# Kernel optimization log

Measured on AMD Instinct MI355X. Metric: run time of the kernel, lower is better.

## Reference

```python
import jax, jax.numpy as jnp
import numpy as np

B, F_IN, D_IN = 1024, 64, 64
N_CAPS, D_CAPS = 32, 64
ROUTINGS = 3
HEADS = 2
EPS = 1e-7  # K.epsilon()


def setup_inputs() -> dict:
    key = jax.random.key(0)
    ks = jax.random.split(key, 8)
    P = N_CAPS * (N_CAPS - 1) // 2
    return {
        "x": jax.random.normal(ks[0], (B, F_IN, D_IN), jnp.float32),
        "reweight_W": jax.random.normal(ks[1], (D_IN, N_CAPS, D_CAPS), jnp.float32) * 0.05,
        "routing_init": 10.0 * jax.random.truncated_normal(ks[2], -2.0, 2.0, (N_CAPS, F_IN), jnp.float32),
        "kernel_fm": jnp.full((N_CAPS, 1), 0.5, jnp.float32),
        "bias_fm": jnp.zeros((D_CAPS,), jnp.float32),
        "kernel_mf": jnp.ones((P, 1), jnp.float32),
        "bias_mf": jnp.zeros((D_CAPS,), jnp.float32),
        "kernel_highint": jnp.full((N_CAPS, 1), 0.5, jnp.float32),
        "bias_highint": jnp.zeros((D_CAPS * HEADS,), jnp.float32),
        "W_query": jax.random.normal(ks[3], (D_CAPS, D_CAPS * HEADS), jnp.float32) * 0.05,
        "W_key": jax.random.normal(ks[4], (D_CAPS, D_CAPS * HEADS), jnp.float32) * 0.05,
        "W_value": jax.random.normal(ks[5], (D_CAPS, D_CAPS * HEADS), jnp.float32) * 0.05,
        "W_res": jax.random.normal(ks[6], (D_CAPS, D_CAPS * HEADS), jnp.float32) * 0.05,
    }


def _squash(v):
    s = jnp.sum(v * v, axis=-1, keepdims=True) + EPS
    return (jnp.sqrt(s) / (0.5 + s)) * v


def _heads(t):
    # [B,N,H*F] -> [H,B,N,F] (matches tf.stack(tf.split(t, H, axis=2)))
    b, n, _ = t.shape
    return t.reshape(b, n, HEADS, D_CAPS).transpose(2, 0, 1, 3)


def reference(x, reweight_W, routing_init, kernel_fm, bias_fm, kernel_mf, bias_mf,
              kernel_highint, bias_highint, W_query, W_key, W_value, W_res):
    # inputs_hat: [B, N, F, C]
    inputs_hat = jnp.einsum('bfd,dnc->bnfc', x, reweight_W)
    b_logits = jnp.broadcast_to(routing_init[None], (x.shape[0], N_CAPS, F_IN))
    for _ in range(ROUTINGS):
        c = jax.nn.softmax(b_logits, axis=1)            # softmax over capsules
        outputs = _squash(jnp.einsum('bnf,bnfc->bnc', c, inputs_hat))
        b_logits = b_logits + jnp.einsum('bnc,bnfc->bnf', outputs, inputs_hat)
    c = jax.nn.softmax(b_logits, axis=1)
    routing_score = c[..., None]                        # [B,N,F,1]
    attention_output = routing_score * inputs_hat       # [B,N,F,C]

    # FM per-field: square-of-sum minus sum-of-square over input capsules
    sum_f = jnp.sum(attention_output, axis=2)           # [B,N,C]
    field_fm = sum_f ** 2 - jnp.sum(attention_output ** 2, axis=2)
    hi_fm = jnp.sum(field_fm * kernel_fm[None], axis=1) + bias_fm  # [B,C]

    field_wise_vectors = sum_f                          # [B,N,C]

    # pairwise MF interactions (itertools.combinations order == triu indices)
    li, ri = np.triu_indices(N_CAPS, k=1)
    emb_prod = field_wise_vectors[:, li] * field_wise_vectors[:, ri]  # [B,P,C]
    h_mf = jnp.sum(emb_prod * kernel_mf[None], axis=1) + bias_mf      # [B,C]

    # InteractingLayer (multi-head self-attention over fields, use_res=True)
    q = _heads(jnp.einsum('bnd,de->bne', field_wise_vectors, W_query))  # [H,B,N,F]
    k = _heads(jnp.einsum('bnd,de->bne', field_wise_vectors, W_key))
    v = _heads(jnp.einsum('bnd,de->bne', field_wise_vectors, W_value))
    attn = jax.nn.softmax(jnp.einsum('hbnf,hbmf->hbnm', q, k), axis=-1)
    out = jnp.einsum('hbnm,hbmf->hbnf', attn, v)        # [H,B,N,F]
    out = out.transpose(1, 2, 0, 3).reshape(x.shape[0], N_CAPS, HEADS * D_CAPS)
    res = jnp.einsum('bnd,de->bne', field_wise_vectors, W_res)
    fv2 = jax.nn.relu(out + res)                        # [B,N,H*F]
    high_int = jnp.sum(fv2 * kernel_highint[None], axis=1) + bias_highint  # [B,2C]

    return jnp.concatenate([hi_fm, h_mf, high_int], axis=-1), routing_score
```

## Files before the change

kernel.cpp:

```cpp
#include <hip/hip_runtime.h>


#define EPS_SQ 1e-7f

typedef __attribute__((ext_vector_type(8))) short bf16x8;
typedef __attribute__((ext_vector_type(4))) float floatx4;

__device__ __forceinline__ int lidx(int r, int c) {
  return r * 68 + ((((c >> 2) ^ (r >> 2)) & 15) << 2) + (c & 3);
}
__device__ __forceinline__ int lidx64(int r, int c) {
  return r * 64 + ((((c >> 2) ^ r ^ (r >> 2)) & 15) << 2) + (c & 3);
}
__device__ __forceinline__ unsigned short f2bf(float f) {
  unsigned u = __float_as_uint(f);
  u += 0x7FFFu + ((u >> 16) & 1u);
  return (unsigned short)(u >> 16);
}

__global__ __launch_bounds__(256) void k_prep2(
    const float* __restrict__ W, const float* __restrict__ Wq,
    const float* __restrict__ Wk, const float* __restrict__ kmf,
    float* __restrict__ Qb, float* __restrict__ Ab, float* __restrict__ Kb)
{
  const int t = threadIdx.x;
  if (blockIdx.x < 32) {
    __shared__ __align__(16) float Mn[64 * 68];
    const int n = blockIdx.x;
#pragma unroll
    for (int k = 0; k < 4; k++) {
      int lin = t + 256 * k; int d = lin >> 4; int c0 = (lin & 15) << 2;
      *(float4*)&Mn[lidx(d, c0)] = *(const float4*)(W + d * 2048 + n * 64 + c0);
    }
    __syncthreads();
    const int d1 = (t >> 4) * 4, d2 = (t & 15) * 4;
    float acc[4][4] = {};
    for (int cq = 0; cq < 64; cq += 4) {
      float m1[4][4], m2[4][4];
#pragma unroll
      for (int i = 0; i < 4; i++) *(float4*)m1[i] = *(const float4*)&Mn[lidx(d1 + i, cq)];
#pragma unroll
      for (int j = 0; j < 4; j++) *(float4*)m2[j] = *(const float4*)&Mn[lidx(d2 + j, cq)];
#pragma unroll
      for (int i = 0; i < 4; i++)
#pragma unroll
        for (int j = 0; j < 4; j++) {
          float s = 0.f;
#pragma unroll
          for (int k = 0; k < 4; k++) s += m1[i][k] * m2[j][k];
          acc[i][j] += s;
        }
    }
#pragma unroll
    for (int i = 0; i < 4; i++)
      *(float4*)(Qb + n * 4096 + (d1 + i) * 64 + d2) = *(float4*)acc[i];
  } else if (blockIdx.x < 40) {
    __shared__ __align__(16) float wkS[64 * 68];
    __shared__ __align__(16) float wqS[16 * 68];
    const int hb = blockIdx.x - 32;
    const int h = hb & 1, rg = hb >> 1;
#pragma unroll
    for (int k = 0; k < 4; k++) {
      int lin = t + 256 * k; int dp = lin >> 4; int e0 = (lin & 15) << 2;
      *(float4*)&wkS[lidx(dp, e0)] = *(const float4*)(Wk + dp * 128 + h * 64 + e0);
    }
    {
      int dl = t >> 4, e0 = (t & 15) << 2;
      *(float4*)&wqS[lidx(dl, e0)] = *(const float4*)(Wq + (rg * 16 + dl) * 128 + h * 64 + e0);
    }
    __syncthreads();
    const int dl = t >> 4, dp0 = (t & 15) << 2;
    float acc[4] = {};
    for (int e = 0; e < 64; e += 4) {
      float q4[4];
      *(float4*)q4 = *(const float4*)&wqS[lidx(dl, e)];
#pragma unroll
      for (int c = 0; c < 4; c++) {
        float mr[4];
        *(float4*)mr = *(const float4*)&wkS[lidx(dp0 + c, e)];
        acc[c] += q4[0] * mr[0] + q4[1] * mr[1] + q4[2] * mr[2] + q4[3] * mr[3];
      }
    }
    *(float4*)(Ab + h * 4096 + (rg * 16 + dl) * 64 + dp0) = *(float4*)acc;
  } else {
    __shared__ float Ks[1024];
    *(float4*)&Ks[t * 4] = make_float4(0.f, 0.f, 0.f, 0.f);
    __syncthreads();
    if (t < 248) {
#pragma unroll
      for (int j = 0; j < 2; j++) {
        int p = t * 2 + j;
        if (p < 496) {
          int l = 0, rem = p;
          while (rem >= 31 - l) { rem -= 31 - l; ++l; }
          int r = l + 1 + rem;
          float v = kmf[p];
          Ks[l * 32 + r] = v;
          Ks[r * 32 + l] = v;
        }
      }
    }
    __syncthreads();
    *(float4*)&Kb[t * 4] = *(const float4*)&Ks[t * 4];
  }
}

__global__ __launch_bounds__(512, 4) void k_route3(
    const float* __restrict__ x, const float* __restrict__ W,
    const float* __restrict__ rinit, const float* __restrict__ Qb,
    float* __restrict__ rs, float* __restrict__ fwv)
{
  __shared__ __align__(16) float smem[2 * 10240];

  const int t = threadIdx.x;
  const int tb = t >> 8, tt = t & 255;
  const int b = blockIdx.x * 2 + tb;

  float* xs  = smem + tb * 10240;
  float* bS  = smem + tb * 10240 + 4096;
  float* cOw = smem + tb * 10240 + 6144;
  float* xcS = smem + tb * 10240 + 8192;

  float* xc0 = smem + 8192;
  float* xc1 = smem + 10240 + 8192;
  float* ow0 = smem + 6144;
  float* ow1 = smem + 10240 + 6144;

#pragma unroll
  for (int k = 0; k < 4; k++) {
    int lin = tt + 256 * k; int f = lin >> 4; int d0 = (lin & 15) << 2;
    *(float4*)&xs[lidx64(f, d0)] = *(const float4*)(x + b * 4096 + f * 64 + d0);
  }
#pragma unroll
  for (int k = 0; k < 2; k++) {
    int lin = tt + 256 * k; int n = lin >> 4; int f0 = (lin & 15) << 2;
    *(float4*)&bS[lidx64(n, f0)] = *(const float4*)(rinit + n * 64 + f0);
  }
  __syncthreads();

  const int tn = tt >> 4, tlo = tt & 15;
  const int nq = t >> 4, sub = t & 15;

  for (int it = 0; it < 4; it++) {
    {
      const int nl = tt & 31, fg = tt >> 5;
#pragma unroll
      for (int qq = 0; qq < 2; qq++) {
        const int f0 = (fg * 2 + qq) * 4;
        float v[4];
        *(float4*)v = *(const float4*)&bS[lidx64(nl, f0)];
        float e[4];
#pragma unroll
        for (int j = 0; j < 4; j++) {
          float m = v[j];
          m = fmaxf(m, __shfl_xor(m, 16, 64));
          m = fmaxf(m, __shfl_xor(m, 8, 64));
          m = fmaxf(m, __shfl_xor(m, 4, 64));
          m = fmaxf(m, __shfl_xor(m, 2, 64));
          m = fmaxf(m, __shfl_xor(m, 1, 64));
          e[j] = __expf(v[j] - m);
          float s = e[j];
          s += __shfl_xor(s, 16, 64);
          s += __shfl_xor(s, 8, 64);
          s += __shfl_xor(s, 4, 64);
          s += __shfl_xor(s, 2, 64);
          s += __shfl_xor(s, 1, 64);
          e[j] /= s;
        }
        *(float4*)&cOw[lidx64(nl, f0)] = *(float4*)e;
      }
    }
    __syncthreads();
    if (it == 3) {
#pragma unroll
      for (int k = 0; k < 2; k++) {
        int lin = tt + 256 * k;
        int n = lin >> 4, fq = lin & 15;
        float4 v = *(const float4*)&cOw[lidx64(n, fq * 4)];
        *(float4*)(rs + b * 2048 + n * 64 + fq * 4) = v;
      }
    }
    {
      const int n0 = tn * 2, d0 = tlo * 4;
      float acc[2][4] = {{0, 0, 0, 0}, {0, 0, 0, 0}};
      for (int fq = 0; fq < 16; fq++) {
        float c0[4], c1[4];
        *(float4*)c0 = *(const float4*)&cOw[lidx64(n0, fq * 4)];
        *(float4*)c1 = *(const float4*)&cOw[lidx64(n0 + 1, fq * 4)];
#pragma unroll
        for (int j = 0; j < 4; j++) {
          float xr[4];
          *(float4*)xr = *(const float4*)&xs[lidx64(fq * 4 + j, d0)];
#pragma unroll
          for (int i = 0; i < 4; i++) {
            acc[0][i] += c0[j] * xr[i];
            acc[1][i] += c1[j] * xr[i];
          }
        }
      }
      *(float4*)&xcS[lidx64(n0, d0)] = *(float4*)acc[0];
      *(float4*)&xcS[lidx64(n0 + 1, d0)] = *(float4*)acc[1];
    }
    __syncthreads();
    if (it == 3) break;

    {
      const float* Qn = Qb + nq * 4096 + sub * 4;
      float y0[4] = {}, y1[4] = {};
#pragma unroll 4
      for (int dq = 0; dq < 16; dq++) {
        float xv0[4], xv1[4];
        *(float4*)xv0 = *(const float4*)&xc0[lidx64(nq, dq * 4)];
        *(float4*)xv1 = *(const float4*)&xc1[lidx64(nq, dq * 4)];
#pragma unroll
        for (int j = 0; j < 4; j++) {
          float4 q = *(const float4*)(Qn + (dq * 4 + j) * 64);
          y0[0] += xv0[j] * q.x; y0[1] += xv0[j] * q.y;
          y0[2] += xv0[j] * q.z; y0[3] += xv0[j] * q.w;
          y1[0] += xv1[j] * q.x; y1[1] += xv1[j] * q.y;
          y1[2] += xv1[j] * q.z; y1[3] += xv1[j] * q.w;
        }
      }
      float xa0[4], xa1[4];
      *(float4*)xa0 = *(const float4*)&xc0[lidx64(nq, sub * 4)];
      *(float4*)xa1 = *(const float4*)&xc1[lidx64(nq, sub * 4)];
      float ps0 = y0[0] * xa0[0] + y0[1] * xa0[1] + y0[2] * xa0[2] + y0[3] * xa0[3];
      float ps1 = y1[0] * xa1[0] + y1[1] * xa1[1] + y1[2] * xa1[2] + y1[3] * xa1[3];
      ps0 += __shfl_xor(ps0, 1, 64); ps0 += __shfl_xor(ps0, 2, 64);
      ps0 += __shfl_xor(ps0, 4, 64); ps0 += __shfl_xor(ps0, 8, 64);
      ps1 += __shfl_xor(ps1, 1, 64); ps1 += __shfl_xor(ps1, 2, 64);
      ps1 += __shfl_xor(ps1, 4, 64); ps1 += __shfl_xor(ps1, 8, 64);
      const float ss0 = ps0 + EPS_SQ, ss1 = ps1 + EPS_SQ;
      const float sc0 = sqrtf(ss0) / (0.5f + ss0);
      const float sc1 = sqrtf(ss1) / (0.5f + ss1);
      float o0[4] = {y0[0] * sc0, y0[1] * sc0, y0[2] * sc0, y0[3] * sc0};
      float o1[4] = {y1[0] * sc1, y1[1] * sc1, y1[2] * sc1, y1[3] * sc1};
      *(float4*)&ow0[lidx64(nq, sub * 4)] = *(float4*)o0;
      *(float4*)&ow1[lidx64(nq, sub * 4)] = *(float4*)o1;
    }
    __syncthreads();

    {
      const int n0 = tn * 2, f0 = tlo * 4;
      float acc[2][4] = {{0, 0, 0, 0}, {0, 0, 0, 0}};
      for (int dq = 0; dq < 64; dq += 4) {
        float o[2][4];
        *(float4*)o[0] = *(const float4*)&cOw[lidx64(n0, dq)];
        *(float4*)o[1] = *(const float4*)&cOw[lidx64(n0 + 1, dq)];
#pragma unroll
        for (int i = 0; i < 4; i++) {
          float xr[4];
          *(float4*)xr = *(const float4*)&xs[lidx64(f0 + i, dq)];
#pragma unroll
          for (int k = 0; k < 4; k++) {
            acc[0][i] += o[0][k] * xr[k];
            acc[1][i] += o[1][k] * xr[k];
          }
        }
      }
#pragma unroll
      for (int j = 0; j < 2; j++) {
        float tmp[4];
        *(float4*)tmp = *(const float4*)&bS[lidx64(n0 + j, f0)];
#pragma unroll
        for (int i = 0; i < 4; i++) tmp[i] += acc[j][i];
        *(float4*)&bS[lidx64(n0 + j, f0)] = *(float4*)tmp;
      }
    }
    __syncthreads();
  }

  {
    const float* Wn = W + nq * 64 + sub * 4;
    float a0[4] = {}, a1[4] = {};
#pragma unroll 4
    for (int dq = 0; dq < 16; dq++) {
      float xv0[4], xv1[4];
      *(float4*)xv0 = *(const float4*)&xc0[lidx64(nq, dq * 4)];
      *(float4*)xv1 = *(const float4*)&xc1[lidx64(nq, dq * 4)];
#pragma unroll
      for (int j = 0; j < 4; j++) {
        float4 w = *(const float4*)(Wn + (dq * 4 + j) * 2048);
        a0[0] += xv0[j] * w.x; a0[1] += xv0[j] * w.y;
        a0[2] += xv0[j] * w.z; a0[3] += xv0[j] * w.w;
        a1[0] += xv1[j] * w.x; a1[1] += xv1[j] * w.y;
        a1[2] += xv1[j] * w.z; a1[3] += xv1[j] * w.w;
      }
    }
    const int b0g = blockIdx.x * 2;
    *(float4*)(fwv + b0g * 2048 + nq * 64 + sub * 4) = *(float4*)a0;
    *(float4*)(fwv + (b0g + 1) * 2048 + nq * 64 + sub * 4) = *(float4*)a1;
  }
}

__global__ __launch_bounds__(256) void k_ih(
    const float* __restrict__ x, const float* __restrict__ W,
    const float* __restrict__ rs, float* __restrict__ ssq)
{
  __shared__ __align__(16) unsigned short xB[4 * 64 * 64];
  __shared__ __align__(16) unsigned short wB[2 * 64 * 64];
  __shared__ unsigned short cF2[4 * 8 * 64];
  const int n_oct = (blockIdx.x & 3) << 3, b0 = (blockIdx.x >> 2) * 4;
  const int t = threadIdx.x, w = t >> 6, lane = t & 63;

#pragma unroll
  for (int k = 0; k < 16; k++) {
    int ch = t + 256 * k;
    int bb = ch >> 10, rem = ch & 1023;
    int f = rem >> 4, fq = rem & 15;
    int dg = fq >> 1, half = fq & 1;
    float4 v = *(const float4*)(x + ((b0 + bb) * 64 + f) * 64 + fq * 4);
    unsigned p0 = f2bf(v.x) | ((unsigned)f2bf(v.y) << 16);
    unsigned p1 = f2bf(v.z) | ((unsigned)f2bf(v.w) << 16);
    *(uint2*)&xB[bb * 4096 + f * 64 + ((dg ^ (f & 7)) << 3) + half * 4] =
        make_uint2(p0, p1);
  }
#pragma unroll
  for (int nn = 0; nn < 8; nn++) {
    float v = rs[(b0 + w) * 2048 + (n_oct + nn) * 64 + lane];
    cF2[(w * 8 + nn) * 64 + lane] = f2bf(v * v);
  }
  __syncthreads();

  const int m = lane & 15, q = lane >> 4, ms = m & 7;
  bf16x8 a[4][2];
#pragma unroll
  for (int mi = 0; mi < 4; mi++) {
    const unsigned short* bp = xB + w * 4096 + (mi * 16 + m) * 64;
#pragma unroll
    for (int kk = 0; kk < 2; kk++)
      a[mi][kk] = *(const bf16x8*)&bp[((kk * 4 + q) ^ ms) << 3];
  }

  for (int np = 0; np < 4; np++) {
    const int n0 = n_oct + np * 2;
    __syncthreads();
    {
      int dd = t >> 2, cq = t & 3;
      int dg = dd >> 3, dl = dd & 7;
#pragma unroll
      for (int nn = 0; nn < 2; nn++) {
        const float* wp = W + dd * 2048 + (n0 + nn) * 64 + cq * 16;
        unsigned short* base = wB + nn * 4096;
#pragma unroll
        for (int i4 = 0; i4 < 4; i4++) {
          float4 v = *(const float4*)(wp + i4 * 4);
          float vv[4] = {v.x, v.y, v.z, v.w};
#pragma unroll
          for (int j = 0; j < 4; j++) {
            int c = cq * 16 + i4 * 4 + j;
            base[c * 64 + ((dg ^ (c & 7)) << 3) + dl] = f2bf(vv[j]);
          }
        }
      }
    }
    __syncthreads();
#pragma unroll
    for (int nn = 0; nn < 2; nn++) {
      bf16x8 bf[4][2];
#pragma unroll
      for (int ci = 0; ci < 4; ci++) {
        const unsigned short* bp = wB + nn * 4096 + (ci * 16 + m) * 64;
#pragma unroll
        for (int kk = 0; kk < 2; kk++)
          bf[ci][kk] = *(const bf16x8*)&bp[((kk * 4 + q) ^ ms) << 3];
      }
      float ps[4] = {0.f, 0.f, 0.f, 0.f};
      const unsigned short* cf = cF2 + (w * 8 + np * 2 + nn) * 64 + q * 4;
#pragma unroll
      for (int mi = 0; mi < 4; mi++) {
        float cfv[4];
#pragma unroll
        for (int r = 0; r < 4; r++)
          cfv[r] = __uint_as_float((unsigned)cf[mi * 16 + r] << 16);
#pragma unroll
        for (int ci = 0; ci < 4; ci++) {
          floatx4 c0 = {0.f, 0.f, 0.f, 0.f};
          c0 = __builtin_amdgcn_mfma_f32_16x16x32_bf16(a[mi][0], bf[ci][0], c0, 0, 0, 0);
          c0 = __builtin_amdgcn_mfma_f32_16x16x32_bf16(a[mi][1], bf[ci][1], c0, 0, 0, 0);
#pragma unroll
          for (int r = 0; r < 4; r++) { float tv = c0[r]; ps[ci] += cfv[r] * tv * tv; }
        }
      }
#pragma unroll
      for (int ci = 0; ci < 4; ci++) {
        ps[ci] += __shfl_xor(ps[ci], 16, 64);
        ps[ci] += __shfl_xor(ps[ci], 32, 64);
      }
      if (q == 0) {
#pragma unroll
        for (int ci = 0; ci < 4; ci++)
          ssq[(b0 + w) * 2048 + (n0 + nn) * 64 + ci * 16 + m] = ps[ci];
      }
    }
  }
}

__global__ __launch_bounds__(256) void k_attn(
    const float* __restrict__ fwv, const float* __restrict__ ssq,
    const float* __restrict__ Ab, const float* __restrict__ Kb,
    const float* __restrict__ Wv, const float* __restrict__ Wr,
    const float* __restrict__ kfm, const float* __restrict__ bfm,
    const float* __restrict__ bmf, const float* __restrict__ khi,
    const float* __restrict__ bhi, float* __restrict__ out0)
{
  __shared__ __align__(16) float smem[8832];
  float* fwS  = smem;
  float* pS   = smem + 2176;
  float* bufA = smem + 4480;
  float* tS   = smem + 6656;
  float* vS   = smem + 4480;
  float* redH = smem + 2176;
  float* Kf   = smem + 4480;
  float* red1 = smem + 5504;

  const int b = blockIdx.x, t = threadIdx.x;
  const int tn = t >> 4, te = t & 15;
  const int n0 = tn * 2, e0 = te * 8, d0 = te * 4;

#pragma unroll
  for (int k = 0; k < 2; k++) {
    int lin = t + 256 * k; int nn = lin >> 4; int c0 = (lin & 15) << 2;
    *(float4*)&fwS[lidx(nn, c0)] = *(const float4*)(fwv + b * 2048 + nn * 64 + c0);
  }
  __syncthreads();

  for (int h = 0; h < 2; h++) {
    float tacc[2][4] = {};
    for (int half = 0; half < 2; half++) {
#pragma unroll
      for (int k = 0; k < 2; k++) {
        int lin = t + 256 * k; int d = lin >> 4; int c0 = (lin & 15) << 2;
        *(float4*)&bufA[lidx(d, c0)] =
            *(const float4*)(Ab + h * 4096 + (half * 32 + d) * 64 + c0);
      }
      __syncthreads();
      for (int dq = 0; dq < 32; dq += 4) {
        float fw0[4], fw1[4];
        *(float4*)fw0 = *(const float4*)&fwS[lidx(n0, half * 32 + dq)];
        *(float4*)fw1 = *(const float4*)&fwS[lidx(n0 + 1, half * 32 + dq)];
#pragma unroll
        for (int j = 0; j < 4; j++) {
          float mr[4];
          *(float4*)mr = *(const float4*)&bufA[lidx(dq + j, d0)];
#pragma unroll
          for (int c = 0; c < 4; c++) {
            tacc[0][c] += fw0[j] * mr[c];
            tacc[1][c] += fw1[j] * mr[c];
          }
        }
      }
      __syncthreads();
    }
    *(float4*)&tS[lidx(n0, d0)] = *(float4*)tacc[0];
    *(float4*)&tS[lidx(n0 + 1, d0)] = *(float4*)tacc[1];
    __syncthreads();
    {
      const int m0 = te * 2;
      float s00 = 0.f, s01 = 0.f, s10 = 0.f, s11 = 0.f;
      for (int kk = 0; kk < 16; kk++) {
        float ta0[4], ta1[4], f0[4], f1[4];
        *(float4*)ta0 = *(const float4*)&tS[lidx(n0, kk * 4)];
        *(float4*)ta1 = *(const float4*)&tS[lidx(n0 + 1, kk * 4)];
        *(float4*)f0 = *(const float4*)&fwS[lidx(m0, kk * 4)];
        *(float4*)f1 = *(const float4*)&fwS[lidx(m0 + 1, kk * 4)];
#pragma unroll
        for (int j = 0; j < 4; j++) {
          s00 += ta0[j] * f0[j]; s01 += ta0[j] * f1[j];
          s10 += ta1[j] * f0[j]; s11 += ta1[j] * f1[j];
        }
      }
      pS[(h * 32 + n0) * 36 + m0] = s00;
      pS[(h * 32 + n0) * 36 + m0 + 1] = s01;
      pS[(h * 32 + n0 + 1) * 36 + m0] = s10;
      pS[(h * 32 + n0 + 1) * 36 + m0 + 1] = s11;
    }
    __syncthreads();
  }

  {
    const int r = t >> 2, sub = t & 3;
    const int base = r * 36 + sub * 8;
    float v0[4], v1[4];
    *(float4*)v0 = *(const float4*)&pS[base];
    *(float4*)v1 = *(const float4*)&pS[base + 4];
    float mx = fmaxf(fmaxf(fmaxf(v0[0], v0[1]), fmaxf(v0[2], v0[3])),
                     fmaxf(fmaxf(v1[0], v1[1]), fmaxf(v1[2], v1[3])));
    mx = fmaxf(mx, __shfl_xor(mx, 1, 64));
    mx = fmaxf(mx, __shfl_xor(mx, 2, 64));
    float sum = 0.f;
#pragma unroll
    for (int j = 0; j < 4; j++) { v0[j] = __expf(v0[j] - mx); sum += v0[j]; }
#pragma unroll
    for (int j = 0; j < 4; j++) { v1[j] = __expf(v1[j] - mx); sum += v1[j]; }
    sum += __shfl_xor(sum, 1, 64);
    sum += __shfl_xor(sum, 2, 64);
    const float inv = 1.0f / sum;
#pragma unroll
    for (int j = 0; j < 4; j++) { v0[j] *= inv; v1[j] *= inv; }
    *(float4*)&pS[base] = *(float4*)v0;
    *(float4*)&pS[base + 4] = *(float4*)v1;
  }
  __syncthreads();

  {
    float acc[2][8] = {};
    for (int dq = 0; dq < 64; dq += 4) {
      float fw0[4], fw1[4];
      *(float4*)fw0 = *(const float4*)&fwS[lidx(n0, dq)];
      *(float4*)fw1 = *(const float4*)&fwS[lidx(n0 + 1, dq)];
#pragma unroll
      for (int jj = 0; jj < 4; jj++) {
        float w8[8];
        *(float4*)&w8[0] = *(const float4*)(Wv + (dq + jj) * 128 + e0);
        *(float4*)&w8[4] = *(const float4*)(Wv + (dq + jj) * 128 + e0 + 4);
#pragma unroll
        for (int j = 0; j < 8; j++) {
          acc[0][j] += fw0[jj] * w8[j];
          acc[1][j] += fw1[jj] * w8[j];
        }
      }
    }
    *(float4*)&vS[n0 * 132 + e0] = *(float4*)&acc[0][0];
    *(float4*)&vS[n0 * 132 + e0 + 4] = *(float4*)&acc[0][4];
    *(float4*)&vS[(n0 + 1) * 132 + e0] = *(float4*)&acc[1][0];
    *(float4*)&vS[(n0 + 1) * 132 + e0 + 4] = *(float4*)&acc[1][4];
  }
  __syncthreads();

  {
    const int h2 = te >> 3;
    float pacc[2][8] = {};
    for (int m = 0; m < 32; m++) {
      float p0 = pS[(h2 * 32 + n0) * 36 + m];
      float p1 = pS[(h2 * 32 + n0 + 1) * 36 + m];
      float vr[8];
      *(float4*)&vr[0] = *(const float4*)&vS[m * 132 + e0];
      *(float4*)&vr[4] = *(const float4*)&vS[m * 132 + e0 + 4];
#pragma unroll
      for (int j = 0; j < 8; j++) {
        pacc[0][j] += p0 * vr[j];
        pacc[1][j] += p1 * vr[j];
      }
    }
    for (int dq = 0; dq < 64; dq += 4) {
      float fw0[4], fw1[4];
      *(float4*)fw0 = *(const float4*)&fwS[lidx(n0, dq)];
      *(float4*)fw1 = *(const float4*)&fwS[lidx(n0 + 1, dq)];
#pragma unroll
      for (int jj = 0; jj < 4; jj++) {
        float w8[8];
        *(float4*)&w8[0] = *(const float4*)(Wr + (dq + jj) * 128 + e0);
        *(float4*)&w8[4] = *(const float4*)(Wr + (dq + jj) * 128 + e0 + 4);
#pragma unroll
        for (int j = 0; j < 8; j++) {
          pacc[0][j] += fw0[jj] * w8[j];
          pacc[1][j] += fw1[jj] * w8[j];
        }
      }
    }
    __syncthreads();
    {
      float kh0 = khi[n0], kh1 = khi[n0 + 1];
      float ph[8];
#pragma unroll
      for (int j = 0; j < 8; j++)
        ph[j] = kh0 * fmaxf(pacc[0][j], 0.f) + kh1 * fmaxf(pacc[1][j], 0.f);
      *(float4*)&redH[tn * 132 + e0] = *(float4*)&ph[0];
      *(float4*)&redH[tn * 132 + e0 + 4] = *(float4*)&ph[4];
    }
  }
  *(float4*)&Kf[t * 4] = *(const float4*)(Kb + t * 4);
  __syncthreads();

  if (t < 128) {
    float s = 0.f;
#pragma unroll
    for (int k = 0; k < 16; k++) s += redH[k * 132 + t];
    out0[b * 256 + 128 + t] = s + bhi[t];
  }
  {
    const int c = t & 63, nq = t >> 6;
    float p = 0.f;
#pragma unroll
    for (int k = 0; k < 8; k++) {
      int nn = nq * 8 + k;
      float fv = fwS[lidx(nn, c)];
      float sv = ssq[b * 2048 + nn * 64 + c];
      p += (fv * fv - sv) * kfm[nn];
    }
    red1[nq * 68 + c] = p;
    float inner[8] = {};
    for (int r = 0; r < 32; r++) {
      float fr = fwS[lidx(r, c)];
#pragma unroll
      for (int l8 = 0; l8 < 8; l8++)
        inner[l8] += Kf[(nq * 8 + l8) * 32 + r] * fr;
    }
    float hmf = 0.f;
#pragma unroll
    for (int l8 = 0; l8 < 8; l8++)
      hmf += fwS[lidx(nq * 8 + l8, c)] * inner[l8];
    red1[(4 + nq) * 68 + c] = hmf;
  }
  __syncthreads();
  if (t < 64) {
    out0[b * 256 + t] = red1[t] + red1[68 + t] + red1[136 + t] + red1[204 + t] + bfm[t];
    float h2 = red1[272 + t] + red1[340 + t] + red1[408 + t] + red1[476 + t];
    out0[b * 256 + 64 + t] = 0.5f * h2 + bmf[t];
  }
}

extern "C" void kernel_launch(void* const* d_in, const int* in_sizes, int n_in,
                              void* d_out, int out_size, void* d_ws, size_t ws_size,
                              hipStream_t stream) {
  (void)in_sizes; (void)n_in; (void)out_size; (void)ws_size;
  const float* x     = (const float*)d_in[0];
  const float* W     = (const float*)d_in[1];
  const float* rinit = (const float*)d_in[2];
  const float* kfm   = (const float*)d_in[3];
  const float* bfm   = (const float*)d_in[4];
  const float* kmf   = (const float*)d_in[5];
  const float* bmf   = (const float*)d_in[6];
  const float* khi   = (const float*)d_in[7];
  const float* bhi   = (const float*)d_in[8];
  const float* Wq    = (const float*)d_in[9];
  const float* Wk    = (const float*)d_in[10];
  const float* Wv    = (const float*)d_in[11];
  const float* Wr    = (const float*)d_in[12];

  float* out0 = (float*)d_out;
  float* rs   = out0 + 1024 * 256;

  float* ws   = (float*)d_ws;
  float* Abuf = ws;
  float* Kbuf = ws + 8192;
  float* Qbuf = ws + 16384;
  float* fwv  = ws + 2097152;
  float* ssq  = ws + 2 * 2097152;

  k_prep2<<<41, 256, 0, stream>>>(W, Wq, Wk, kmf, Qbuf, Abuf, Kbuf);
  k_route3<<<512, 512, 0, stream>>>(x, W, rinit, Qbuf, rs, fwv);
  k_ih<<<1024, 256, 0, stream>>>(x, W, rs, ssq);
  k_attn<<<1024, 256, 0, stream>>>(fwv, ssq, Abuf, Kbuf, Wv, Wr,
                                   kfm, bfm, bmf, khi, bhi, out0);
}
```

Measured before the change: 260.1 us.

## Process four batch rows per routing block with split-K partial sums

```diff
diff --git a/kernel.cpp b/kernel.cpp
--- a/kernel.cpp
+++ b/kernel.cpp
@@ -105,26 +105,24 @@
   }
 }
 
-__global__ __launch_bounds__(512, 4) void k_route3(
+__global__ __launch_bounds__(1024) void k_route4(
     const float* __restrict__ x, const float* __restrict__ W,
     const float* __restrict__ rinit, const float* __restrict__ Qb,
     float* __restrict__ rs, float* __restrict__ fwv)
 {
-  __shared__ __align__(16) float smem[2 * 10240];
+  __shared__ __align__(16) float smem[4 * 8192];
 
   const int t = threadIdx.x;
   const int tb = t >> 8, tt = t & 255;
-  const int b = blockIdx.x * 2 + tb;
-
-  float* xs  = smem + tb * 10240;
-  float* bS  = smem + tb * 10240 + 4096;
-  float* cOw = smem + tb * 10240 + 6144;
-  float* xcS = smem + tb * 10240 + 8192;
-
-  float* xc0 = smem + 8192;
-  float* xc1 = smem + 10240 + 8192;
-  float* ow0 = smem + 6144;
-  float* ow1 = smem + 10240 + 6144;
+  const int b = blockIdx.x * 4 + tb;
+
+  float* xs = smem + tb * 8192;
+  float* bS = xs + 4096;
+  float* wk = xs + 6144;
+
+  float* wkp[4];
+#pragma unroll
+  for (int bb = 0; bb < 4; bb++) wkp[bb] = smem + bb * 8192 + 6144;
 
 #pragma unroll
   for (int k = 0; k < 4; k++) {
@@ -139,7 +137,7 @@
   __syncthreads();
 
   const int tn = tt >> 4, tlo = tt & 15;
-  const int nq = t >> 4, sub = t & 15;
+  const int nq = (t >> 4) & 31, sub = t & 15, p = t >> 9;
 
   for (int it = 0; it < 4; it++) {
     {
@@ -167,7 +165,7 @@
           s += __shfl_xor(s, 1, 64);
           e[j] /= s;
         }
-        *(float4*)&cOw[lidx64(nl, f0)] = *(float4*)e;
+        *(float4*)&wk[lidx64(nl, f0)] = *(float4*)e;
       }
     }
     __syncthreads();
@@ -176,17 +174,18 @@
       for (int k = 0; k < 2; k++) {
         int lin = tt + 256 * k;
         int n = lin >> 4, fq = lin & 15;
-        float4 v = *(const float4*)&cOw[lidx64(n, fq * 4)];
+        float4 v = *(const float4*)&wk[lidx64(n, fq * 4)];
         *(float4*)(rs + b * 2048 + n * 64 + fq * 4) = v;
       }
+      __syncthreads();
     }
     {
       const int n0 = tn * 2, d0 = tlo * 4;
       float acc[2][4] = {{0, 0, 0, 0}, {0, 0, 0, 0}};
       for (int fq = 0; fq < 16; fq++) {
         float c0[4], c1[4];
-        *(float4*)c0 = *(const float4*)&cOw[lidx64(n0, fq * 4)];
-        *(float4*)c1 = *(const float4*)&cOw[lidx64(n0 + 1, fq * 4)];
+        *(float4*)c0 = *(const float4*)&wk[lidx64(n0, fq * 4)];
+        *(float4*)c1 = *(const float4*)&wk[lidx64(n0 + 1, fq * 4)];
 #pragma unroll
         for (int j = 0; j < 4; j++) {
           float xr[4];
@@ -198,55 +197,75 @@
           }
         }
       }
-      *(float4*)&xcS[lidx64(n0, d0)] = *(float4*)acc[0];
-      *(float4*)&xcS[lidx64(n0 + 1, d0)] = *(float4*)acc[1];
+      *(float4*)&wk[lidx64(n0, d0)] = *(float4*)acc[0];
+      *(float4*)&wk[lidx64(n0 + 1, d0)] = *(float4*)acc[1];
     }
     __syncthreads();
     if (it == 3) break;
 
     {
-      const float* Qn = Qb + nq * 4096 + sub * 4;
-      float y0[4] = {}, y1[4] = {};
+      const float* Qn = Qb + nq * 4096 + p * 32 * 64 + sub * 4;
+      float y[4][4] = {};
 #pragma unroll 4
-      for (int dq = 0; dq < 16; dq++) {
-        float xv0[4], xv1[4];
-        *(float4*)xv0 = *(const float4*)&xc0[lidx64(nq, dq * 4)];
-        *(float4*)xv1 = *(const float4*)&xc1[lidx64(nq, dq * 4)];
+      for (int dq = 0; dq < 8; dq++) {
+        const int c0 = p * 32 + dq * 4;
+        float xv[4][4];
+#pragma unroll
+        for (int bb = 0; bb < 4; bb++)
+          *(float4*)xv[bb] = *(const float4*)&wkp[bb][lidx64(nq, c0)];
 #pragma unroll
         for (int j = 0; j < 4; j++) {
           float4 q = *(const float4*)(Qn + (dq * 4 + j) * 64);
-          y0[0] += xv0[j] * q.x; y0[1] += xv0[j] * q.y;
-          y0[2] += xv0[j] * q.z; y0[3] += xv0[j] * q.w;
-          y1[0] += xv1[j] * q.x; y1[1] += xv1[j] * q.y;
-          y1[2] += xv1[j] * q.z; y1[3] += xv1[j] * q.w;
-        }
-      }
-      float xa0[4], xa1[4];
-      *(float4*)xa0 = *(const float4*)&xc0[lidx64(nq, sub * 4)];
-      *(float4*)xa1 = *(const float4*)&xc1[lidx64(nq, sub * 4)];
-      float ps0 = y0[0] * xa0[0] + y0[1] * xa0[1] + y0[2] * xa0[2] + y0[3] * xa0[3];
-      float ps1 = y1[0] * xa1[0] + y1[1] * xa1[1] + y1[2] * xa1[2] + y1[3] * xa1[3];
-      ps0 += __shfl_xor(ps0, 1, 64); ps0 += __shfl_xor(ps0, 2, 64);
-      ps0 += __shfl_xor(ps0, 4, 64); ps0 += __shfl_xor(ps0, 8, 64);
-      ps1 += __shfl_xor(ps1, 1, 64); ps1 += __shfl_xor(ps1, 2, 64);
-      ps1 += __shfl_xor(ps1, 4, 64); ps1 += __shfl_xor(ps1, 8, 64);
-      const float ss0 = ps0 + EPS_SQ, ss1 = ps1 + EPS_SQ;
-      const float sc0 = sqrtf(ss0) / (0.5f + ss0);
-      const float sc1 = sqrtf(ss1) / (0.5f + ss1);
-      float o0[4] = {y0[0] * sc0, y0[1] * sc0, y0[2] * sc0, y0[3] * sc0};
-      float o1[4] = {y1[0] * sc1, y1[1] * sc1, y1[2] * sc1, y1[3] * sc1};
-      *(float4*)&ow0[lidx64(nq, sub * 4)] = *(float4*)o0;
-      *(float4*)&ow1[lidx64(nq, sub * 4)] = *(float4*)o1;
-    }
-    __syncthreads();
+#pragma unroll
+          for (int bb = 0; bb < 4; bb++) {
+            y[bb][0] += xv[bb][j] * q.x; y[bb][1] += xv[bb][j] * q.y;
+            y[bb][2] += xv[bb][j] * q.z; y[bb][3] += xv[bb][j] * q.w;
+          }
+        }
+      }
+      float xa[4][4];
+      if (p == 0) {
+#pragma unroll
+        for (int bb = 0; bb < 4; bb++)
+          *(float4*)xa[bb] = *(const float4*)&wkp[bb][lidx64(nq, sub * 4)];
+      }
+      __syncthreads();
+      if (p == 1) {
+#pragma unroll
+        for (int bb = 0; bb < 4; bb++)
+          *(float4*)&wkp[bb][lidx64(nq, sub * 4)] = *(float4*)y[bb];
+      }
+      __syncthreads();
+      if (p == 0) {
+#pragma unroll
+        for (int bb = 0; bb < 4; bb++) {
+          float pt[4];
+          *(float4*)pt = *(const float4*)&wkp[bb][lidx64(nq, sub * 4)];
+          y[bb][0] += pt[0]; y[bb][1] += pt[1];
+          y[bb][2] += pt[2]; y[bb][3] += pt[3];
+        }
+#pragma unroll
+        for (int bb = 0; bb < 4; bb++) {
+          float s = y[bb][0] * xa[bb][0] + y[bb][1] * xa[bb][1]
+                  + y[bb][2] * xa[bb][2] + y[bb][3] * xa[bb][3];
+          s += __shfl_xor(s, 1, 64); s += __shfl_xor(s, 2, 64);
+          s += __shfl_xor(s, 4, 64); s += __shfl_xor(s, 8, 64);
+          const float ss = s + EPS_SQ;
+          const float sc = sqrtf(ss) / (0.5f + ss);
+          float o[4] = {y[bb][0] * sc, y[bb][1] * sc, y[bb][2] * sc, y[bb][3] * sc};
+          *(float4*)&wkp[bb][lidx64(nq, sub * 4)] = *(float4*)o;
+        }
+      }
+      __syncthreads();
+    }
 
     {
       const int n0 = tn * 2, f0 = tlo * 4;
       float acc[2][4] = {{0, 0, 0, 0}, {0, 0, 0, 0}};
       for (int dq = 0; dq < 64; dq += 4) {
         float o[2][4];
-        *(float4*)o[0] = *(const float4*)&cOw[lidx64(n0, dq)];
-        *(float4*)o[1] = *(const float4*)&cOw[lidx64(n0 + 1, dq)];
+        *(float4*)o[0] = *(const float4*)&wk[lidx64(n0, dq)];
+        *(float4*)o[1] = *(const float4*)&wk[lidx64(n0 + 1, dq)];
 #pragma unroll
         for (int i = 0; i < 4; i++) {
           float xr[4];
@@ -271,25 +290,43 @@
   }
 
   {
-    const float* Wn = W + nq * 64 + sub * 4;
-    float a0[4] = {}, a1[4] = {};
+    const float* Wn = W + (p * 32) * 2048 + nq * 64 + sub * 4;
+    float a[4][4] = {};
 #pragma unroll 4
-    for (int dq = 0; dq < 16; dq++) {
-      float xv0[4], xv1[4];
-      *(float4*)xv0 = *(const float4*)&xc0[lidx64(nq, dq * 4)];
-      *(float4*)xv1 = *(const float4*)&xc1[lidx64(nq, dq * 4)];
+    for (int dq = 0; dq < 8; dq++) {
+      const int c0 = p * 32 + dq * 4;
+      float xv[4][4];
+#pragma unroll
+      for (int bb = 0; bb < 4; bb++)
+        *(float4*)xv[bb] = *(const float4*)&wkp[bb][lidx64(nq, c0)];
 #pragma unroll
       for (int j = 0; j < 4; j++) {
         float4 w = *(const float4*)(Wn + (dq * 4 + j) * 2048);
-        a0[0] += xv0[j] * w.x; a0[1] += xv0[j] * w.y;
-        a0[2] += xv0[j] * w.z; a0[3] += xv0[j] * w.w;
-        a1[0] += xv1[j] * w.x; a1[1] += xv1[j] * w.y;
-        a1[2] += xv1[j] * w.z; a1[3] += xv1[j] * w.w;
-      }
-    }
-    const int b0g = blockIdx.x * 2;
-    *(float4*)(fwv + b0g * 2048 + nq * 64 + sub * 4) = *(float4*)a0;
-    *(float4*)(fwv + (b0g + 1) * 2048 + nq * 64 + sub * 4) = *(float4*)a1;
+#pragma unroll
+        for (int bb = 0; bb < 4; bb++) {
+          a[bb][0] += xv[bb][j] * w.x; a[bb][1] += xv[bb][j] * w.y;
+          a[bb][2] += xv[bb][j] * w.z; a[bb][3] += xv[bb][j] * w.w;
+        }
+      }
+    }
+    __syncthreads();
+    if (p == 1) {
+#pragma unroll
+      for (int bb = 0; bb < 4; bb++)
+        *(float4*)&wkp[bb][lidx64(nq, sub * 4)] = *(float4*)a[bb];
+    }
+    __syncthreads();
+    if (p == 0) {
+      const int b0g = blockIdx.x * 4;
+#pragma unroll
+      for (int bb = 0; bb < 4; bb++) {
+        float pt[4];
+        *(float4*)pt = *(const float4*)&wkp[bb][lidx64(nq, sub * 4)];
+        a[bb][0] += pt[0]; a[bb][1] += pt[1];
+        a[bb][2] += pt[2]; a[bb][3] += pt[3];
+        *(float4*)(fwv + (b0g + bb) * 2048 + nq * 64 + sub * 4) = *(float4*)a[bb];
+      }
+    }
   }
 }
 
@@ -640,7 +677,7 @@
   float* ssq  = ws + 2 * 2097152;
 
   k_prep2<<<41, 256, 0, stream>>>(W, Wq, Wk, kmf, Qbuf, Abuf, Kbuf);
-  k_route3<<<512, 512, 0, stream>>>(x, W, rinit, Qbuf, rs, fwv);
+  k_route4<<<256, 1024, 0, stream>>>(x, W, rinit, Qbuf, rs, fwv);
   k_ih<<<1024, 256, 0, stream>>>(x, W, rs, ssq);
   k_attn<<<1024, 256, 0, stream>>>(fwv, ssq, Abuf, Kbuf, Wv, Wr,
                                    kfm, bfm, bmf, khi, bhi, out0);
```

After: 289.2 us. 11.2% more time.
